# Kernel tuning notes

Hardware: AMD Instinct MI355X
Metric: run time of the kernel (lower is better)

The kernel has to match this reference:

```python
import jax, jax.numpy as jnp
import numpy as np

B, CIN, COUT, H, W, LAT, G = 4, 128, 256, 64, 64, 256, 16
EPS = 1e-5


def _bn(x, p):
    # p: [4, C] stacked (gamma, beta, running_mean, running_var); eval-mode BN over channel dim 1
    g, b, m, v = p
    sh = (1, -1) + (1,) * (x.ndim - 2)
    return (x - m.reshape(sh)) * (g.reshape(sh) * jax.lax.rsqrt(v.reshape(sh) + EPS)) + b.reshape(sh)


def _prelu(x, a):
    return jnp.where(x > 0, x, a * x)


def _pool(x):
    b, c, h, w = x.shape
    return x.reshape(b, c, h // 2, 2, w // 2, 2).mean((3, 5))


def _conv1x1(w, x):
    return jnp.einsum('oc,bchw->bohw', w, x)


def _cbn(x, latent, bnp, lin):
    y = _bn(x, bnp)
    sb = latent @ lin.T  # [B, 2C]
    s, b = jnp.split(sb, 2, axis=-1)
    return y * s[:, :, None, None] + b[:, :, None, None]


def _axial(x, wqkv, bn_qkv, bn_sim, bn_out, rel, dim):
    # x: [B, C, H, W]; attend along H (dim==0) or W (dim==1)
    x = x.transpose(0, 3, 1, 2) if dim == 0 else x.transpose(0, 2, 1, 3)
    b, d1, c, s = x.shape
    x = x.reshape(b * d1, c, s)
    qkv = _bn(jnp.einsum('oc,bcs->bos', wqkv, x), bn_qkv)  # [bN, 2*COUT, S]
    gc = COUT // G
    qkv = qkv.reshape(b * d1, G, 2 * gc, s)
    q, k, v = qkv[:, :, :gc // 2], qkv[:, :, gc // 2:gc], qkv[:, :, gc:]
    idx = jnp.arange(s)[:, None] - jnp.arange(s)[None, :] + s - 1
    emb = rel[:, idx]  # [2*gc, S, S]
    qe, ke, ve = emb[:gc // 2], emb[gc // 2:gc], emb[gc:]
    q_emb = jnp.einsum('bgci,cij->bgij', q, qe)
    k_emb = jnp.einsum('bgci,cij->bgij', k, ke)
    # torch reinterprets [b,g,S,S] as 'bgci': contraction over the 3rd axis
    qk = jnp.einsum('bgki,bgkj->bgij', q_emb, k_emb)
    sim = jnp.concatenate([qk, q_emb, k_emb], axis=1)  # [bN, 3G, S, S]
    sim = _bn(sim, bn_sim)
    sim = sim.reshape(b * d1, 3, G, s, s).sum(1)
    sim = jax.nn.softmax(sim, axis=-1)
    att = jnp.einsum('bgij,bgcj->bgci', sim, v)
    att_e = jnp.einsum('bgij,cij->bgci', sim, ve)
    o = jnp.stack([att, att_e], axis=3).reshape(b * d1, 2 * COUT, s)
    o = _bn(o, bn_out)
    o = o.reshape(b, d1, COUT, 2, s).sum(3)
    return o.transpose(0, 2, 3, 1) if dim == 0 else o.transpose(0, 2, 1, 3)


def _bn_params(key, c):
    k1, k2, k3, k4 = jax.random.split(key, 4)
    return jnp.stack([1.0 + 0.1 * jax.random.normal(k1, (c,)),
                      0.1 * jax.random.normal(k2, (c,)),
                      0.05 * jax.random.normal(k3, (c,)),
                      jax.random.uniform(k4, (c,), minval=0.5, maxval=1.5)])


def setup_inputs() -> dict:
    key = jax.random.key(0)
    ks = list(jax.random.split(key, 24))
    gc = COUT // G
    inp = {
        'x': jax.random.normal(ks[0], (B, CIN, H, W), dtype=jnp.float32),
        'latent': jax.random.normal(ks[1], (B, LAT), dtype=jnp.float32),
        'w_in': 0.1 * jax.random.normal(ks[2], (COUT, CIN)),
        'bn_in': _bn_params(ks[3], COUT),
        'lin_in': 0.1 * jax.random.normal(ks[4], (2 * COUT, LAT)),
        'alpha_in': jnp.array(0.25, dtype=jnp.float32),
        'a0_wqkv': 0.1 * jax.random.normal(ks[5], (2 * COUT, COUT)),
        'a0_bn_qkv': _bn_params(ks[6], 2 * COUT),
        'a0_bn_sim': _bn_params(ks[7], 3 * G),
        'a0_bn_out': _bn_params(ks[8], 2 * COUT),
        'a0_rel': 0.1 * jax.random.normal(ks[9], (2 * gc, 2 * H - 1)),
        'a1_wqkv': 0.1 * jax.random.normal(ks[10], (2 * COUT, COUT)),
        'a1_bn_qkv': _bn_params(ks[11], 2 * COUT),
        'a1_bn_sim': _bn_params(ks[12], 3 * G),
        'a1_bn_out': _bn_params(ks[13], 2 * COUT),
        'a1_rel': 0.1 * jax.random.normal(ks[14], (2 * gc, 2 * W - 1)),
        'w_out': 0.1 * jax.random.normal(ks[15], (COUT, COUT)),
        'bn_out': _bn_params(ks[16], COUT),
        'lin_out': 0.1 * jax.random.normal(ks[17], (2 * COUT, LAT)),
        'w_res': 0.1 * jax.random.normal(ks[18], (COUT, CIN)),
        'alpha_fin': jnp.array(0.25, dtype=jnp.float32),
    }
    return inp


def reference(x, latent, w_in, bn_in, lin_in, alpha_in,
              a0_wqkv, a0_bn_qkv, a0_bn_sim, a0_bn_out, a0_rel,
              a1_wqkv, a1_bn_qkv, a1_bn_sim, a1_bn_out, a1_rel,
              w_out, bn_out, lin_out, w_res, alpha_fin):
    out = _prelu(_cbn(_conv1x1(w_in, x), latent, bn_in, lin_in), alpha_in)
    out = _axial(out, a0_wqkv, a0_bn_qkv, a0_bn_sim, a0_bn_out, a0_rel, 0)
    out = _axial(out, a1_wqkv, a1_bn_qkv, a1_bn_sim, a1_bn_out, a1_rel, 1)
    out = _cbn(_conv1x1(w_out, _pool(out)), latent, bn_out, lin_out)
    out = out + _pool(_conv1x1(w_res, x))
    return _prelu(out, alpha_fin)
```

## Files before the change

kernel.cpp:

```cpp
#include <hip/hip_runtime.h>
#include <hip/hip_bf16.h>

#define EPS_F 1e-5f

typedef __attribute__((ext_vector_type(8))) _Float16 f16x8;
typedef __attribute__((ext_vector_type(4))) _Float16 f16x4;
typedef __attribute__((ext_vector_type(4))) float f32x4;

union U16x8 { ushort u[8]; _Float16 h[8]; f16x8 v; };
union U16x4 { ushort u[4]; f16x4 v; };

static __device__ inline ushort f2h(float f) {
  _Float16 h = (_Float16)f;
  return __builtin_bit_cast(ushort, h);
}
static __device__ inline float h2f(ushort u) {
  return (float)__builtin_bit_cast(_Float16, u);
}

__global__ void __launch_bounds__(256) prep_kernel(
    const float* __restrict__ w_in, const float* __restrict__ a0w,
    const float* __restrict__ a1w, const float* __restrict__ w_out,
    const float* __restrict__ w_res,
    const float* __restrict__ latent, const float* __restrict__ lin_in,
    const float* __restrict__ lin_out,
    const float* __restrict__ a0_rel, const float* __restrict__ a1_rel,
    const float* __restrict__ x,
    ushort* __restrict__ w16, ushort* __restrict__ relimg,
    float* __restrict__ sb_in, float* __restrict__ sb_out,
    ushort* __restrict__ x16, ushort* __restrict__ pool_x) {
  const int gid = blockIdx.x;
  const int tid = threadIdx.x;
  __shared__ __align__(16) char lsm[10240];

  if (gid < 1588) {
    int idx = gid * 256 + tid;
    if (idx < 393216) {
      const float* src; int off;
      if (idx < 32768)       { src = w_in;  off = 0; }
      else if (idx < 163840) { src = a0w;   off = 32768; }
      else if (idx < 294912) { src = a1w;   off = 163840; }
      else if (idx < 360448) { src = w_out; off = 294912; }
      else                   { src = w_res; off = 360448; }
      w16[idx] = f2h(src[idx - off]);
    } else if (idx < 397312) {
      int r = idx - 393216;
      int which = r >> 11;
      int rr = r & 2047;
      int b = rr >> 9, k = rr & 511;
      const float* lin = which ? lin_out : lin_in;
      const float* lv = latent + b * 256;
      const float* lr = lin + k * 256;
      float acc = 0.f;
#pragma unroll 8
      for (int l = 0; l < 256; ++l) acc += lv[l] * lr[l];
      (which ? sb_out : sb_in)[b * 512 + k] = acc;
    } else if (idx < 406528) {
      int e = idx - 397312;
      int which = e >= 4608;
      int s = which ? e - 4608 : e;
      const float* rel = which ? a1_rel : a0_rel;
      ushort val = 0;
      if (s < 2560) {
        int d = s / 20, c = s % 20;
        if (c < 16 && d < 127) val = f2h(rel[c * 127 + d]);
      } else {
        int pos = (s - 2560) * 2;
        int c = pos >> 8;
        int inner = (pos & 255) ^ ((c & 7) << 4);
        int d = inner >> 1;
        if (d < 127) val = f2h(rel[(16 + c) * 127 + d]);
      }
      relimg[which * 4608 + s] = val;
    }
  } else if (gid < 2100) {
    int e = gid - 1588;
    int pt = e & 31, ct = (e >> 5) & 3, b = e >> 7;
    ushort (*Lt)[40] = (ushort(*)[40])lsm;
#pragma unroll
    for (int r = 0; r < 16; ++r) {
      int e2 = tid + 256 * r;
      int c = e2 >> 7, p = e2 & 127;
      Lt[p][c] = f2h(x[((size_t)(b * 128 + ct * 32 + c)) * 4096 + pt * 128 + p]);
    }
    __syncthreads();
#pragma unroll
    for (int r = 0; r < 2; ++r) {
      int e2 = tid + 256 * r;
      int p = e2 >> 2, q = e2 & 3;
      *(f16x8*)&x16[((size_t)b * 4096 + pt * 128 + p) * 128 + ct * 32 + 8 * q] =
          *(const f16x8*)&Lt[p][8 * q];
    }
  } else {
    int e = gid - 2100;
    int ip = e & 31, ct = (e >> 5) & 3, b = e >> 7;
    float (*Lp)[33] = (float(*)[33])lsm;
    {
      int c = tid >> 3, grp = tid & 7;
      const float* base = x + ((size_t)(b * 128 + ct * 32 + c)) * 4096 + (2 * ip) * 64 + 8 * grp;
      float4 a0 = *(const float4*)&base[0];
      float4 a1 = *(const float4*)&base[4];
      float4 b0 = *(const float4*)&base[64];
      float4 b1 = *(const float4*)&base[68];
      Lp[c][4 * grp + 0] = 0.25f * (a0.x + a0.y + b0.x + b0.y);
      Lp[c][4 * grp + 1] = 0.25f * (a0.z + a0.w + b0.z + b0.w);
      Lp[c][4 * grp + 2] = 0.25f * (a1.x + a1.y + b1.x + b1.y);
      Lp[c][4 * grp + 3] = 0.25f * (a1.z + a1.w + b1.z + b1.w);
    }
    __syncthreads();
    {
      int jp = tid >> 3, q = tid & 7;
      ushort4 o;
      o.x = f2h(Lp[4 * q + 0][jp]);
      o.y = f2h(Lp[4 * q + 1][jp]);
      o.z = f2h(Lp[4 * q + 2][jp]);
      o.w = f2h(Lp[4 * q + 3][jp]);
      *(ushort4*)&pool_x[((size_t)b * 1024 + ip * 32 + jp) * 128 + ct * 32 + 4 * q] = o;
    }
  }
}

template <int MODE>
__global__ void __launch_bounds__(256) conv_mfma_kernel(
    const ushort* __restrict__ X, const ushort* __restrict__ W16,
    ushort* __restrict__ Y16, int Cin, int Cout, int P,
    const float* __restrict__ bn, const float* __restrict__ sb,
    const float* __restrict__ alpha) {
  const int tid = threadIdx.x;
  const int p0 = blockIdx.x * 64;
  const int o0 = blockIdx.y * 64;
  const int b  = blockIdx.z;
  const int lane = tid & 63;
  const int wv = tid >> 6;
  const int m = lane & 15, h = lane >> 4;
  const int wr = wv >> 1, wc = wv & 1;

  __shared__ __align__(16) char smem[18432];
  ushort (*Xs)[72] = (ushort(*)[72])smem;
  ushort (*Ws)[72] = (ushort(*)[72])(smem + 9216);
  ushort (*Es)[72] = (ushort(*)[72])smem;

  f32x4 acc[2][2];
#pragma unroll
  for (int i = 0; i < 2; ++i)
#pragma unroll
    for (int j = 0; j < 2; ++j) acc[i][j] = (f32x4){0.f, 0.f, 0.f, 0.f};

  const ushort* Xb = X + (size_t)b * P * Cin;

  for (int k0 = 0; k0 < Cin; k0 += 64) {
    __syncthreads();
#pragma unroll
    for (int r = 0; r < 2; ++r) {
      int e = tid + 256 * r;
      int pp = e >> 3, ch = e & 7;
      *(f16x8*)&Xs[pp][8 * ch] =
          *(const f16x8*)&Xb[(size_t)(p0 + pp) * Cin + k0 + 8 * ch];
    }
#pragma unroll
    for (int r = 0; r < 2; ++r) {
      int e = tid + 256 * r;
      int oc = e >> 3, ch = e & 7;
      *(f16x8*)&Ws[oc][8 * ch] =
          *(const f16x8*)&W16[(size_t)(o0 + oc) * Cin + k0 + 8 * ch];
    }
    __syncthreads();
#pragma unroll
    for (int ks = 0; ks < 2; ++ks) {
      f16x8 af[2], bf[2];
#pragma unroll
      for (int t = 0; t < 2; ++t) af[t] = *(const f16x8*)&Ws[32 * wr + 16 * t + m][32 * ks + 8 * h];
#pragma unroll
      for (int t = 0; t < 2; ++t) bf[t] = *(const f16x8*)&Xs[32 * wc + 16 * t + m][32 * ks + 8 * h];
#pragma unroll
      for (int ta = 0; ta < 2; ++ta)
#pragma unroll
        for (int tb = 0; tb < 2; ++tb)
          acc[ta][tb] = __builtin_amdgcn_mfma_f32_16x16x32_f16(af[ta], bf[tb], acc[ta][tb], 0, 0, 0);
    }
  }

  float scl[2][4], shf[2][4];
#pragma unroll
  for (int ta = 0; ta < 2; ++ta)
#pragma unroll
    for (int r = 0; r < 4; ++r) {
      int oc = o0 + 32 * wr + 16 * ta + 4 * h + r;
      float scale = 1.f, shift = 0.f;
      if (MODE & 1) {
        float sc = bn[oc] * rsqrtf(bn[3 * Cout + oc] + EPS_F);
        scale = sc;
        shift = bn[Cout + oc] - bn[2 * Cout + oc] * sc;
      }
      if (MODE & 2) {
        float ss = sb[b * 2 * Cout + oc];
        float bb = sb[b * 2 * Cout + Cout + oc];
        scale *= ss;
        shift = shift * ss + bb;
      }
      scl[ta][r] = scale; shf[ta][r] = shift;
    }
  float al = (MODE & 8) ? *alpha : 0.f;

  __syncthreads();
#pragma unroll
  for (int ta = 0; ta < 2; ++ta)
#pragma unroll
    for (int tb = 0; tb < 2; ++tb)
#pragma unroll
      for (int r = 0; r < 4; ++r) {
        float v = acc[ta][tb][r] * scl[ta][r] + shf[ta][r];
        if (MODE & 8) v = v > 0.f ? v : al * v;
        Es[32 * wc + 16 * tb + m][32 * wr + 16 * ta + 4 * h + r] = f2h(v);
      }
  __syncthreads();
#pragma unroll
  for (int r = 0; r < 2; ++r) {
    int e = tid + 256 * r;
    int pp = e >> 3, q = e & 7;
    *(f16x8*)&Y16[((size_t)b * P + p0 + pp) * Cout + o0 + 8 * q] =
        *(const f16x8*)&Es[pp][8 * q];
  }
}

__global__ void __launch_bounds__(256) final_fused_kernel(
    const ushort* __restrict__ t0, const ushort* __restrict__ pool_x,
    const ushort* __restrict__ Wo, const ushort* __restrict__ Wr,
    float* __restrict__ Y32,
    const float* __restrict__ bn, const float* __restrict__ sb,
    const float* __restrict__ alpha) {
  const int tid = threadIdx.x;
  const int p0 = blockIdx.x * 64;
  const int o0 = blockIdx.y * 64;
  const int b  = blockIdx.z;
  const int lane = tid & 63;
  const int wv = tid >> 6;
  const int m = lane & 15, h = lane >> 4;
  const int wr = wv >> 1, wc = wv & 1;

  __shared__ __align__(16) char smem[18432];
  ushort (*Xs)[72] = (ushort(*)[72])smem;
  ushort (*Ws)[72] = (ushort(*)[72])(smem + 9216);

  f32x4 acc1[2][2], acc2[2][2];
#pragma unroll
  for (int i = 0; i < 2; ++i)
#pragma unroll
    for (int j = 0; j < 2; ++j) {
      acc1[i][j] = (f32x4){0.f, 0.f, 0.f, 0.f};
      acc2[i][j] = (f32x4){0.f, 0.f, 0.f, 0.f};
    }

  for (int k0 = 0; k0 < 256; k0 += 64) {
    __syncthreads();
#pragma unroll
    for (int r = 0; r < 2; ++r) {
      int e = tid + 256 * r;
      int pp = e >> 3, ch = e & 7;
      int pg = p0 + pp;
      int ip = pg >> 5, jp = pg & 31;
      size_t tb = ((size_t)b * 4096 + ip * 128 + jp * 2) * 256 + k0 + 8 * ch;
      U16x8 a, bb, c, d, o;
      a.v  = *(const f16x8*)&t0[tb];
      bb.v = *(const f16x8*)&t0[tb + 256];
      c.v  = *(const f16x8*)&t0[tb + 64 * 256];
      d.v  = *(const f16x8*)&t0[tb + 65 * 256];
#pragma unroll
      for (int e2 = 0; e2 < 8; ++e2)
        o.h[e2] = ((a.h[e2] + bb.h[e2]) + (c.h[e2] + d.h[e2])) * (_Float16)0.25f;
      *(f16x8*)&Xs[pp][8 * ch] = o.v;
    }
#pragma unroll
    for (int r = 0; r < 2; ++r) {
      int e = tid + 256 * r;
      int oc = e >> 3, ch = e & 7;
      *(f16x8*)&Ws[oc][8 * ch] = *(const f16x8*)&Wo[(size_t)(o0 + oc) * 256 + k0 + 8 * ch];
    }
    __syncthreads();
#pragma unroll
    for (int ks = 0; ks < 2; ++ks) {
      f16x8 af[2], bf[2];
#pragma unroll
      for (int t = 0; t < 2; ++t) af[t] = *(const f16x8*)&Ws[32 * wr + 16 * t + m][32 * ks + 8 * h];
#pragma unroll
      for (int t = 0; t < 2; ++t) bf[t] = *(const f16x8*)&Xs[32 * wc + 16 * t + m][32 * ks + 8 * h];
#pragma unroll
      for (int ta = 0; ta < 2; ++ta)
#pragma unroll
        for (int tb2 = 0; tb2 < 2; ++tb2)
          acc1[ta][tb2] = __builtin_amdgcn_mfma_f32_16x16x32_f16(af[ta], bf[tb2], acc1[ta][tb2], 0, 0, 0);
    }
  }

  for (int k0 = 0; k0 < 128; k0 += 64) {
    __syncthreads();
#pragma unroll
    for (int r = 0; r < 2; ++r) {
      int e = tid + 256 * r;
      int pp = e >> 3, ch = e & 7;
      *(f16x8*)&Xs[pp][8 * ch] =
          *(const f16x8*)&pool_x[((size_t)b * 1024 + p0 + pp) * 128 + k0 + 8 * ch];
    }
#pragma unroll
    for (int r = 0; r < 2; ++r) {
      int e = tid + 256 * r;
      int oc = e >> 3, ch = e & 7;
      *(f16x8*)&Ws[oc][8 * ch] = *(const f16x8*)&Wr[(size_t)(o0 + oc) * 128 + k0 + 8 * ch];
    }
    __syncthreads();
#pragma unroll
    for (int ks = 0; ks < 2; ++ks) {
      f16x8 af[2], bf[2];
#pragma unroll
      for (int t = 0; t < 2; ++t) af[t] = *(const f16x8*)&Ws[32 * wr + 16 * t + m][32 * ks + 8 * h];
#pragma unroll
      for (int t = 0; t < 2; ++t) bf[t] = *(const f16x8*)&Xs[32 * wc + 16 * t + m][32 * ks + 8 * h];
#pragma unroll
      for (int ta = 0; ta < 2; ++ta)
#pragma unroll
        for (int tb2 = 0; tb2 < 2; ++tb2)
          acc2[ta][tb2] = __builtin_amdgcn_mfma_f32_16x16x32_f16(af[ta], bf[tb2], acc2[ta][tb2], 0, 0, 0);
    }
  }

  const float al = *alpha;
#pragma unroll
  for (int ta = 0; ta < 2; ++ta)
#pragma unroll
    for (int r = 0; r < 4; ++r) {
      int oc = o0 + 32 * wr + 16 * ta + 4 * h + r;
      float sc = bn[oc] * rsqrtf(bn[768 + oc] + EPS_F);
      float shift = bn[256 + oc] - bn[512 + oc] * sc;
      float ss = sb[b * 512 + oc];
      float bb = sb[b * 512 + 256 + oc];
      float scale = sc * ss;
      shift = shift * ss + bb;
#pragma unroll
      for (int tb2 = 0; tb2 < 2; ++tb2) {
        int p = p0 + 32 * wc + 16 * tb2 + m;
        float v = acc1[ta][tb2][r] * scale + shift + acc2[ta][tb2][r];
        v = v > 0.f ? v : al * v;
        Y32[((size_t)b * 256 + oc) * 1024 + p] = v;
      }
    }
}

__global__ void __launch_bounds__(256) axial_attn_kernel(
    const ushort* __restrict__ t0in, const ushort* __restrict__ wqkv,
    const float* __restrict__ bn_qkv,
    const ushort* __restrict__ relimg,
    const float* __restrict__ bn_sim, const float* __restrict__ bn_out,
    ushort* __restrict__ out16) {
  const int tid = threadIdx.x;
  int lin = blockIdx.x;
  int wg = ((lin & 7) << 9) + (lin >> 3);
  const int g  = wg & 15;
  const int bd = wg >> 4;
  const int b  = bd >> 6;
  const int d1 = bd & 63;

  __shared__ __align__(16) char smem[32768];
#define RAA(d, c)  (smem + (d) * 40 + (c) * 2)
#define QKA(i, c)  (smem + 5120 + (i) * 48 + (c) * 2)
#define QEA(i, k)  (smem + 8192 + (i) * 144 + (k) * 2)
#define KEA(j, k)  (smem + 17408 + (j) * 144 + (k) * 2)
#define VCA(c, j)  (smem + 26624 + ((((c) * 128 + (j) * 2)) ^ (((c) & 7) << 4)))
#define RVA(c, d)  (smem + 28672 + ((((c) * 256 + (d) * 2)) ^ (((c) & 7) << 4)))
#define A2A(i, d)  (smem + (i) * 272 + (d) * 2)

  const int lane = tid & 63;
  const int wv   = tid >> 6;
  const int m    = lane & 15;
  const int h    = lane >> 4;
  const int wr   = wv >> 1, wc = wv & 1;

  {
    const uint4* img = (const uint4*)relimg;
    ((uint4*)smem)[tid] = img[tid];
    if (tid < 64) ((uint4*)smem)[256 + tid] = img[256 + tid];
    ((uint4*)(smem + 28672))[tid] = img[320 + tid];
  }

  f32x4 cacc[2];
  cacc[0] = (f32x4){0.f, 0.f, 0.f, 0.f};
  cacc[1] = (f32x4){0.f, 0.f, 0.f, 0.f};
  {
    const ushort* Xb = t0in + ((size_t)b * 4096 + d1) * 256;
    const ushort* Wg = wqkv + ((size_t)(g * 32 + 16 * wr + m)) * 256;
    char* const XS0 = smem + 8192;
    char* const XS1 = smem + 17408;
    const int si = tid >> 3, ssub = tid & 7;
#pragma unroll
    for (int r = 0; r < 2; ++r) {
      int i = si + 32 * r;
      *(f16x8*)(XS0 + i * 144 + ssub * 16) =
          *(const f16x8*)&Xb[(size_t)i * 16384 + 8 * ssub];
    }
    __syncthreads();
#pragma unroll
    for (int c = 0; c < 4; ++c) {
      char* cur = (c & 1) ? XS1 : XS0;
      if (c < 3) {
        char* nxt = (c & 1) ? XS0 : XS1;
#pragma unroll
        for (int r = 0; r < 2; ++r) {
          int i = si + 32 * r;
          *(f16x8*)(nxt + i * 144 + ssub * 16) =
              *(const f16x8*)&Xb[(size_t)i * 16384 + (c + 1) * 64 + 8 * ssub];
        }
      }
#pragma unroll
      for (int ks = 0; ks < 2; ++ks) {
        f16x8 af = *(const f16x8*)&Wg[c * 64 + 32 * ks + 8 * h];
#pragma unroll
        for (int tb = 0; tb < 2; ++tb) {
          int i = 32 * wc + 16 * tb + m;
          f16x8 bf = *(const f16x8*)(cur + i * 144 + (32 * ks + 8 * h) * 2);
          cacc[tb] = __builtin_amdgcn_mfma_f32_16x16x32_f16(af, bf, cacc[tb], 0, 0, 0);
        }
      }
      __syncthreads();
    }
  }
  {
    float scl[4], shf[4];
#pragma unroll
    for (int r = 0; r < 4; ++r) {
      int ch = g * 32 + 16 * wr + 4 * h + r;
      float sc = bn_qkv[ch] * rsqrtf(bn_qkv[1536 + ch] + EPS_F);
      scl[r] = sc;
      shf[r] = bn_qkv[512 + ch] - bn_qkv[1024 + ch] * sc;
    }
    if (wr == 0) {
#pragma unroll
      for (int tb = 0; tb < 2; ++tb) {
        int i = 32 * wc + 16 * tb + m;
        U16x4 o;
#pragma unroll
        for (int r = 0; r < 4; ++r) o.u[r] = f2h(cacc[tb][r] * scl[r] + shf[r]);
        *(f16x4*)QKA(i, 4 * h) = o.v;
      }
    } else {
#pragma unroll
      for (int tb = 0; tb < 2; ++tb) {
        int i = 32 * wc + 16 * tb + m;
#pragma unroll
        for (int r = 0; r < 4; ++r)
          *(ushort*)VCA(4 * h + r, i) = f2h(cacc[tb][r] * scl[r] + shf[r]);
      }
    }
  }
  __syncthreads();

  {
    const int nt = wv;
    const int n = 16 * nt + m;
    f16x4 bqk = *(const f16x4*)QKA(n, 4 * h);
    const f16x4 z4 = (f16x4){(_Float16)0.f, (_Float16)0.f, (_Float16)0.f, (_Float16)0.f};
    const bool qside = (h < 2);
#pragma unroll
    for (int k = 0; k < 5; ++k) {
      int dt = nt + k;
      f16x4 ar = *(const f16x4*)RAA(16 * dt + m, 4 * h);
      f16x4 arQ = qside ? ar : z4;
      f16x4 arK = qside ? z4 : ar;
      f32x4 dq = __builtin_amdgcn_mfma_f32_16x16x16f16(arQ, bqk, (f32x4){0.f,0.f,0.f,0.f}, 0, 0, 0);
      f32x4 dk = __builtin_amdgcn_mfma_f32_16x16x16f16(arK, bqk, (f32x4){0.f,0.f,0.f,0.f}, 0, 0, 0);
#pragma unroll
      for (int r = 0; r < 4; ++r) {
        int d = 16 * dt + 4 * h + r;
        int i = n - d + 63;
        if (k == 0 || k == 4) {
          if ((unsigned)i < 64u) {
            *(ushort*)QEA(i, n) = f2h(dq[r]);
            *(ushort*)KEA(i, n) = f2h(dk[r]);
          }
        } else {
          *(ushort*)QEA(i, n) = f2h(dq[r]);
          *(ushort*)KEA(i, n) = f2h(dk[r]);
        }
      }
    }
  }
  __syncthreads();

  f32x4 acc[4];
#pragma unroll
  for (int tj = 0; tj < 4; ++tj) acc[tj] = (f32x4){0.f, 0.f, 0.f, 0.f};
  {
    const int ia = 16 * wv + m;
    f16x8 af0 = *(const f16x8*)QEA(ia, 8 * h);
    f16x8 af1 = *(const f16x8*)QEA(ia, 32 + 8 * h);
#pragma unroll
    for (int tj = 0; tj < 4; ++tj) {
      int j = 16 * tj + m;
      f16x8 bf0 = *(const f16x8*)KEA(j, 8 * h);
      f16x8 bf1 = *(const f16x8*)KEA(j, 32 + 8 * h);
      acc[tj] = __builtin_amdgcn_mfma_f32_16x16x32_f16(af0, bf0, acc[tj], 0, 0, 0);
      acc[tj] = __builtin_amdgcn_mfma_f32_16x16x32_f16(af1, bf1, acc[tj], 0, 0, 0);
    }
  }

  float s_qk = bn_sim[g]      * rsqrtf(bn_sim[144 + g] + EPS_F);
  float s_qe = bn_sim[16 + g] * rsqrtf(bn_sim[160 + g] + EPS_F);
  float s_ke = bn_sim[32 + g] * rsqrtf(bn_sim[176 + g] + EPS_F);
  float sh   = (bn_sim[48 + g] - bn_sim[96 + g]  * s_qk)
             + (bn_sim[64 + g] - bn_sim[112 + g] * s_qe)
             + (bn_sim[80 + g] - bn_sim[128 + g] * s_ke);

  const int ib = 16 * wv + 4 * h;
  float sv[4][4];
#pragma unroll
  for (int tj = 0; tj < 4; ++tj) {
    int j = 16 * tj + m;
    f16x4 qe4 = *(const f16x4*)QEA(j, ib);
    f16x4 ke4 = *(const f16x4*)KEA(j, ib);
#pragma unroll
    for (int r = 0; r < 4; ++r)
      sv[tj][r] = acc[tj][r] * s_qk + (float)qe4[r] * s_qe + (float)ke4[r] * s_ke + sh;
  }

  float p[4][4];
  {
    float mx[4];
#pragma unroll
    for (int r = 0; r < 4; ++r) {
      float v = fmaxf(fmaxf(sv[0][r], sv[1][r]), fmaxf(sv[2][r], sv[3][r]));
      v = fmaxf(v, __shfl_xor(v, 1));
      v = fmaxf(v, __shfl_xor(v, 2));
      v = fmaxf(v, __shfl_xor(v, 4));
      v = fmaxf(v, __shfl_xor(v, 8));
      mx[r] = v;
    }
#pragma unroll
    for (int r = 0; r < 4; ++r) {
      float ssum = 0.f;
#pragma unroll
      for (int tj = 0; tj < 4; ++tj) {
        p[tj][r] = __expf(sv[tj][r] - mx[r]);
        ssum += p[tj][r];
      }
      ssum += __shfl_xor(ssum, 1);
      ssum += __shfl_xor(ssum, 2);
      ssum += __shfl_xor(ssum, 4);
      ssum += __shfl_xor(ssum, 8);
      float inv = 1.f / ssum;
#pragma unroll
      for (int tj = 0; tj < 4; ++tj) p[tj][r] *= inv;
    }
  }

  __syncthreads();

  {
    uint4 z = make_uint4(0u, 0u, 0u, 0u);
    uint4* base = (uint4*)(smem + wv * 4352);
#pragma unroll
    for (int u = 0; u < 4; ++u) base[lane + 64 * u] = z;
    if (lane < 16) base[lane + 256] = z;
  }
#pragma unroll
  for (int tj = 0; tj < 4; ++tj) {
    int j = 16 * tj + m;
#pragma unroll
    for (int r = 0; r < 4; ++r) {
      int i = ib + r;
      *(ushort*)A2A(i, i - j + 63) = f2h(p[tj][r]);
    }
  }

  f32x4 accA = (f32x4){0.f, 0.f, 0.f, 0.f};
  f32x4 accE = (f32x4){0.f, 0.f, 0.f, 0.f};
  {
    const int ia = 16 * wv + m;
#pragma unroll
    for (int ks = 0; ks < 2; ++ks) {
      U16x8 pa;
#pragma unroll
      for (int e = 0; e < 8; ++e) {
        int j = 32 * ks + 8 * h + e;
        pa.u[e] = *(ushort*)A2A(ia, ia - j + 63);
      }
      f16x8 vb = *(const f16x8*)VCA(m, 32 * ks + 8 * h);
      accA = __builtin_amdgcn_mfma_f32_16x16x32_f16(pa.v, vb, accA, 0, 0, 0);
    }
#pragma unroll
    for (int ks = 0; ks < 4; ++ks) {
      f16x8 pe = *(const f16x8*)A2A(ia, 32 * ks + 8 * h);
      f16x8 rv = *(const f16x8*)RVA(m, 32 * ks + 8 * h);
      accE = __builtin_amdgcn_mfma_f32_16x16x32_f16(pe, rv, accE, 0, 0, 0);
    }
  }

  {
    int oc = g * 16 + m;
    int c0 = 2 * oc, c1 = c0 + 1;
    float sc0 = bn_out[c0] * rsqrtf(bn_out[1536 + c0] + EPS_F);
    float sh0 = bn_out[512 + c0] - bn_out[1024 + c0] * sc0;
    float sc1 = bn_out[c1] * rsqrtf(bn_out[1536 + c1] + EPS_F);
    float sh1 = bn_out[512 + c1] - bn_out[1024 + c1] * sc1;
    float vv[4];
    vv[0] = accA[0] * sc0 + accE[0] * sc1 + sh0 + sh1;
    vv[1] = accA[1] * sc0 + accE[1] * sc1 + sh0 + sh1;
    vv[2] = accA[2] * sc0 + accE[2] * sc1 + sh0 + sh1;
    vv[3] = accA[3] * sc0 + accE[3] * sc1 + sh0 + sh1;
    size_t base = ((size_t)b * 4096 + (size_t)d1 * 64 + ib) * 256 + oc;
#pragma unroll
    for (int r = 0; r < 4; ++r)
      out16[base + (size_t)r * 256] = f2h(vv[r]);
  }
#undef RAA
#undef QKA
#undef QEA
#undef KEA
#undef VCA
#undef RVA
#undef A2A
}

extern "C" void kernel_launch(void* const* d_in, const int* in_sizes, int n_in,
                              void* d_out, int out_size, void* d_ws, size_t ws_size,
                              hipStream_t stream) {
  const float* x         = (const float*)d_in[0];
  const float* latent    = (const float*)d_in[1];
  const float* w_in      = (const float*)d_in[2];
  const float* bn_in     = (const float*)d_in[3];
  const float* lin_in    = (const float*)d_in[4];
  const float* alpha_in  = (const float*)d_in[5];
  const float* a0_wqkv   = (const float*)d_in[6];
  const float* a0_bn_qkv = (const float*)d_in[7];
  const float* a0_bn_sim = (const float*)d_in[8];
  const float* a0_bn_out = (const float*)d_in[9];
  const float* a0_rel    = (const float*)d_in[10];
  const float* a1_wqkv   = (const float*)d_in[11];
  const float* a1_bn_qkv = (const float*)d_in[12];
  const float* a1_bn_sim = (const float*)d_in[13];
  const float* a1_bn_out = (const float*)d_in[14];
  const float* a1_rel    = (const float*)d_in[15];
  const float* w_out     = (const float*)d_in[16];
  const float* bn_outp   = (const float*)d_in[17];
  const float* lin_out   = (const float*)d_in[18];
  const float* w_res     = (const float*)d_in[19];
  const float* alpha_fin = (const float*)d_in[20];

  float* ws = (float*)d_ws;
  float* sb_in  = ws;
  float* sb_out = ws + 2048;
  ushort* w16   = (ushort*)(ws + 4096);
  ushort* relimg = w16 + 393216;
  ushort* x16   = relimg + 9216;
  ushort* t0    = x16 + 2097152;
  ushort* t1    = t0 + 4194304;
  ushort* pool_x = t1 + 4194304;

  ushort* w_in16  = w16;
  ushort* a0w16   = w16 + 32768;
  ushort* a1w16   = w16 + 163840;
  ushort* w_out16 = w16 + 294912;
  ushort* w_res16 = w16 + 360448;
  ushort* rimg_a  = relimg;
  ushort* rimg_b  = relimg + 4608;

  prep_kernel<<<2612, 256, 0, stream>>>(w_in, a0_wqkv, a1_wqkv, w_out, w_res,
                                        latent, lin_in, lin_out, a0_rel, a1_rel,
                                        x, w16, relimg, sb_in, sb_out, x16, pool_x);

  conv_mfma_kernel<11><<<dim3(64, 4, 4), 256, 0, stream>>>(
      x16, w_in16, t0, 128, 256, 4096, bn_in, sb_in, alpha_in);

  axial_attn_kernel<<<4096, 256, 0, stream>>>(
      t0, a0w16, a0_bn_qkv, rimg_a, a0_bn_sim, a0_bn_out, t1);

  axial_attn_kernel<<<4096, 256, 0, stream>>>(
      t1, a1w16, a1_bn_qkv, rimg_b, a1_bn_sim, a1_bn_out, t0);

  final_fused_kernel<<<dim3(16, 4, 4), 256, 0, stream>>>(
      t0, pool_x, w_out16, w_res16, (float*)d_out, bn_outp, sb_out, alpha_fin);
}
```

Baseline: 120.5 us.

## Fuse input pooling into fp16 transpose blocks and raise wave priority around MFMA

The separate prep blocks that re-read x to compute the 2x2-pooled input are removed. Pooling is now computed from the fp16 transposed tile already in LDS, which cuts 512 blocks and a second full read of x. Separately, s_setprio(1)/s_setprio(0) pairs are wrapped around the MFMA loops in the conv, final and attention kernels to favour matrix-issuing waves. Pooling now averages fp16-rounded values instead of fp32 ones, which slightly changes numerics.

```diff
diff --git a/kernel.cpp b/kernel.cpp
--- a/kernel.cpp
+++ b/kernel.cpp
@@ -73,7 +73,7 @@
       }
       relimg[which * 4608 + s] = val;
     }
-  } else if (gid < 2100) {
+  } else {
     int e = gid - 1588;
     int pt = e & 31, ct = (e >> 5) & 3, b = e >> 7;
     ushort (*Lt)[40] = (ushort(*)[40])lsm;
@@ -91,31 +91,17 @@
       *(f16x8*)&x16[((size_t)b * 4096 + pt * 128 + p) * 128 + ct * 32 + 8 * q] =
           *(const f16x8*)&Lt[p][8 * q];
     }
-  } else {
-    int e = gid - 2100;
-    int ip = e & 31, ct = (e >> 5) & 3, b = e >> 7;
-    float (*Lp)[33] = (float(*)[33])lsm;
-    {
-      int c = tid >> 3, grp = tid & 7;
-      const float* base = x + ((size_t)(b * 128 + ct * 32 + c)) * 4096 + (2 * ip) * 64 + 8 * grp;
-      float4 a0 = *(const float4*)&base[0];
-      float4 a1 = *(const float4*)&base[4];
-      float4 b0 = *(const float4*)&base[64];
-      float4 b1 = *(const float4*)&base[68];
-      Lp[c][4 * grp + 0] = 0.25f * (a0.x + a0.y + b0.x + b0.y);
-      Lp[c][4 * grp + 1] = 0.25f * (a0.z + a0.w + b0.z + b0.w);
-      Lp[c][4 * grp + 2] = 0.25f * (a1.x + a1.y + b1.x + b1.y);
-      Lp[c][4 * grp + 3] = 0.25f * (a1.z + a1.w + b1.z + b1.w);
-    }
-    __syncthreads();
     {
       int jp = tid >> 3, q = tid & 7;
       ushort4 o;
-      o.x = f2h(Lp[4 * q + 0][jp]);
-      o.y = f2h(Lp[4 * q + 1][jp]);
-      o.z = f2h(Lp[4 * q + 2][jp]);
-      o.w = f2h(Lp[4 * q + 3][jp]);
-      *(ushort4*)&pool_x[((size_t)b * 1024 + ip * 32 + jp) * 128 + ct * 32 + 4 * q] = o;
+#pragma unroll
+      for (int cc = 0; cc < 4; ++cc) {
+        int c = 4 * q + cc;
+        float v = 0.25f * (h2f(Lt[2 * jp][c]) + h2f(Lt[2 * jp + 1][c]) +
+                           h2f(Lt[64 + 2 * jp][c]) + h2f(Lt[64 + 2 * jp + 1][c]));
+        ((ushort*)&o)[cc] = f2h(v);
+      }
+      *(ushort4*)&pool_x[((size_t)b * 1024 + pt * 32 + jp) * 128 + ct * 32 + 4 * q] = o;
     }
   }
 }
@@ -165,6 +151,7 @@
           *(const f16x8*)&W16[(size_t)(o0 + oc) * Cin + k0 + 8 * ch];
     }
     __syncthreads();
+    __builtin_amdgcn_s_setprio(1);
 #pragma unroll
     for (int ks = 0; ks < 2; ++ks) {
       f16x8 af[2], bf[2];
@@ -178,6 +165,7 @@
         for (int tb = 0; tb < 2; ++tb)
           acc[ta][tb] = __builtin_amdgcn_mfma_f32_16x16x32_f16(af[ta], bf[tb], acc[ta][tb], 0, 0, 0);
     }
+    __builtin_amdgcn_s_setprio(0);
   }
 
   float scl[2][4], shf[2][4];
@@ -277,6 +265,7 @@
       *(f16x8*)&Ws[oc][8 * ch] = *(const f16x8*)&Wo[(size_t)(o0 + oc) * 256 + k0 + 8 * ch];
     }
     __syncthreads();
+    __builtin_amdgcn_s_setprio(1);
 #pragma unroll
     for (int ks = 0; ks < 2; ++ks) {
       f16x8 af[2], bf[2];
@@ -290,6 +279,7 @@
         for (int tb2 = 0; tb2 < 2; ++tb2)
           acc1[ta][tb2] = __builtin_amdgcn_mfma_f32_16x16x32_f16(af[ta], bf[tb2], acc1[ta][tb2], 0, 0, 0);
     }
+    __builtin_amdgcn_s_setprio(0);
   }
 
   for (int k0 = 0; k0 < 128; k0 += 64) {
@@ -308,6 +298,7 @@
       *(f16x8*)&Ws[oc][8 * ch] = *(const f16x8*)&Wr[(size_t)(o0 + oc) * 128 + k0 + 8 * ch];
     }
     __syncthreads();
+    __builtin_amdgcn_s_setprio(1);
 #pragma unroll
     for (int ks = 0; ks < 2; ++ks) {
       f16x8 af[2], bf[2];
@@ -321,6 +312,7 @@
         for (int tb2 = 0; tb2 < 2; ++tb2)
           acc2[ta][tb2] = __builtin_amdgcn_mfma_f32_16x16x32_f16(af[ta], bf[tb2], acc2[ta][tb2], 0, 0, 0);
     }
+    __builtin_amdgcn_s_setprio(0);
   }
 
   const float al = *alpha;
@@ -409,6 +401,7 @@
               *(const f16x8*)&Xb[(size_t)i * 16384 + (c + 1) * 64 + 8 * ssub];
         }
       }
+      __builtin_amdgcn_s_setprio(1);
 #pragma unroll
       for (int ks = 0; ks < 2; ++ks) {
         f16x8 af = *(const f16x8*)&Wg[c * 64 + 32 * ks + 8 * h];
@@ -419,6 +412,7 @@
           cacc[tb] = __builtin_amdgcn_mfma_f32_16x16x32_f16(af, bf, cacc[tb], 0, 0, 0);
         }
       }
+      __builtin_amdgcn_s_setprio(0);
       __syncthreads();
     }
   }
@@ -458,6 +452,7 @@
     f16x4 bqk = *(const f16x4*)QKA(n, 4 * h);
     const f16x4 z4 = (f16x4){(_Float16)0.f, (_Float16)0.f, (_Float16)0.f, (_Float16)0.f};
     const bool qside = (h < 2);
+    __builtin_amdgcn_s_setprio(1);
 #pragma unroll
     for (int k = 0; k < 5; ++k) {
       int dt = nt + k;
@@ -481,6 +476,7 @@
         }
       }
     }
+    __builtin_amdgcn_s_setprio(0);
   }
   __syncthreads();
 
@@ -491,6 +487,7 @@
     const int ia = 16 * wv + m;
     f16x8 af0 = *(const f16x8*)QEA(ia, 8 * h);
     f16x8 af1 = *(const f16x8*)QEA(ia, 32 + 8 * h);
+    __builtin_amdgcn_s_setprio(1);
 #pragma unroll
     for (int tj = 0; tj < 4; ++tj) {
       int j = 16 * tj + m;
@@ -499,6 +496,7 @@
       acc[tj] = __builtin_amdgcn_mfma_f32_16x16x32_f16(af0, bf0, acc[tj], 0, 0, 0);
       acc[tj] = __builtin_amdgcn_mfma_f32_16x16x32_f16(af1, bf1, acc[tj], 0, 0, 0);
     }
+    __builtin_amdgcn_s_setprio(0);
   }
 
   float s_qk = bn_sim[g]      * rsqrtf(bn_sim[144 + g] + EPS_F);
@@ -573,6 +571,7 @@
   f32x4 accE = (f32x4){0.f, 0.f, 0.f, 0.f};
   {
     const int ia = 16 * wv + m;
+    __builtin_amdgcn_s_setprio(1);
 #pragma unroll
     for (int ks = 0; ks < 2; ++ks) {
       U16x8 pa;
@@ -590,6 +589,7 @@
       f16x8 rv = *(const f16x8*)RVA(m, 32 * ks + 8 * h);
       accE = __builtin_amdgcn_mfma_f32_16x16x32_f16(pe, rv, accE, 0, 0, 0);
     }
+    __builtin_amdgcn_s_setprio(0);
   }
 
   {
@@ -661,7 +661,7 @@
   ushort* rimg_a  = relimg;
   ushort* rimg_b  = relimg + 4608;
 
-  prep_kernel<<<2612, 256, 0, stream>>>(w_in, a0_wqkv, a1_wqkv, w_out, w_res,
+  prep_kernel<<<2100, 256, 0, stream>>>(w_in, a0_wqkv, a1_wqkv, w_out, w_res,
                                         latent, lin_in, lin_out, a0_rel, a1_rel,
                                         x, w16, relimg, sb_in, sb_out, x16, pool_x);
 
```

Result: slower. 123.7 us (+2.6%).
